# Kernel optimization log

Hardware: AMD Instinct MI355X
Metric: run time of the kernel (lower is better)

The kernel has to match this reference:

```python
import jax, jax.numpy as jnp
import numpy as np

# ---- constants matching init_kwargs ----
LAMBDA_CON = 0.4
LAMBDA_BC = 0.2
DX = 0.01
DT = 0.001
U0 = 1.0
VISC = 0.01
CROP = 512
N = CROP - 2  # 510
B = 32

# ---- fixed-weight convs expressed as slicing stencils (valid conv) ----
def div_ddx(x):      # 3x3 kernel [[0,0,0],[-1,1,0],[0,0,0]]
    return x[:, :, 1:-1, 1:-1] - x[:, :, 1:-1, :-2]

def div_ddy(x):      # 3x3 kernel [[0,-1,0],[0,1,0],[0,0,0]]
    return x[:, :, 1:-1, 1:-1] - x[:, :, :-2, 1:-1]

def avg_x(x):        # 2x2 kernel [[.5,.5],[0,0]]
    return 0.5 * (x[:, :, :-1, :-1] + x[:, :, :-1, 1:])

def avg_y(x):        # 2x2 kernel [[.5,0],[.5,0]]
    return 0.5 * (x[:, :, :-1, :-1] + x[:, :, 1:, :-1])

def up_ddx(x):       # 2x2 kernel [[-1,1],[0,0]]
    return x[:, :, :-1, 1:] - x[:, :, :-1, :-1]

def up_ddy(x):       # 2x2 kernel [[-1,0],[1,0]]
    return x[:, :, 1:, :-1] - x[:, :, :-1, :-1]

def down_ddx(x):     # 2x2 kernel [[0,0],[-1,1]]
    return x[:, :, 1:, 1:] - x[:, :, 1:, :-1]

def down_ddy(x):     # 2x2 kernel [[0,-1],[0,1]]
    return x[:, :, 1:, 1:] - x[:, :, :-1, 1:]

def laplacian(x):    # 3x3 kernel [[0,-1,0],[-1,4,-1],[0,-1,0]]
    return (4.0 * x[:, :, 1:-1, 1:-1]
            - x[:, :, 1:-1, 2:] - x[:, :, 1:-1, :-2]
            - x[:, :, 2:, 1:-1] - x[:, :, :-2, 1:-1])


def _poisson_dudt(u, v, p):
    ue = avg_x(u)
    vn = avg_x(v)
    flux_e = ue * avg_x(u) - (VISC / DX) * up_ddx(u)
    flux_n = vn * avg_y(u) - (VISC / DX) * up_ddy(u)
    flux_e = flux_e[:, :, :, :-1]
    flux_n = flux_n[:, :, :, :-1]
    pu = p[:, :, :-1, 1:-1]
    return (-down_ddx(flux_e) - down_ddy(flux_n) - down_ddx(pu)) / DX


def _poisson_dvdt(u, v, p):
    ue = avg_y(u)
    vn = avg_y(v)
    flux_e = ue * avg_x(v) - (VISC / DX) * up_ddx(v)
    flux_n = vn * avg_y(v) - (VISC / DX) * up_ddy(v)
    flux_e = flux_e[:, :, :-1, :]
    flux_n = flux_n[:, :, :-1, :]
    pv = p[:, :, 1:-1, :-1]
    return (-down_ddx(flux_e) - down_ddy(flux_n) - down_ddy(pv)) / DX


def _bc_loss(g):
    u, v, p = g[:, 0], g[:, 1], g[:, 2]  # [B,H,W]
    y0 = (jnp.sum(u[:, 0, 1:N] + u[:, 1, 1:N], axis=1)
          + jnp.sum(v[:, 0, 1:N + 1] + p[:, 0, 1:N + 1], axis=1))
    yL = (jnp.sum(2.0 * U0 - (u[:, N, 1:N] + u[:, N + 1, 1:N]), axis=1)
          + jnp.sum(v[:, N + 1, 1:N + 1] + p[:, N + 1, 1:N + 1], axis=1))
    x0 = (jnp.sum(v[:, 1:N, 0] + v[:, 1:N, 1], axis=1)
          + jnp.sum(u[:, 1:N + 1, 0] + p[:, 1:N + 1, 0], axis=1))
    xL = (jnp.sum(v[:, 1:N, N + 1] + v[:, 1:N, N], axis=1)
          + jnp.sum(u[:, 1:N + 1, N + 1] + p[:, 1:N + 1, N + 1], axis=1))
    return jnp.sum(jnp.abs(y0) + jnp.abs(yL) + jnp.abs(x0) + jnp.abs(xL))


def setup_inputs() -> dict:
    key = jax.random.key(0)
    k1, k2 = jax.random.split(key)
    gen_output = jax.random.normal(k1, (B, 3, CROP, CROP), dtype=jnp.float32)
    p_next_step = jax.random.normal(k2, (B, 1, CROP, CROP), dtype=jnp.float32)
    return {"gen_output": gen_output, "p_next_step": p_next_step}


def reference(gen_output, p_next_step):
    u = gen_output[:, 0:1]
    v = gen_output[:, 1:2]
    p = gen_output[:, 2:3]

    # continuity residual on interior grid [B,1,N,N]
    continuity_res = (div_ddx(u) + div_ddy(v)) / DX
    continuity_loss = jnp.mean(jnp.abs(continuity_res), axis=(2, 3))  # [B,1]

    dudt = _poisson_dudt(u, v, p)  # [B,1,N,N-1]
    dvdt = _poisson_dvdt(u, v, p)  # [B,1,N-1,N]
    dudt_pad = jnp.pad(dudt, ((0, 0), (0, 0), (1, 1), (1, 2)))  # -> [B,1,CROP,CROP]
    dvdt_pad = jnp.pad(dvdt, ((0, 0), (0, 0), (1, 2), (1, 1)))

    p_prime = p_next_step - p
    u_new = u + dudt_pad * DT
    v_new = v + dvdt_pad * DT
    b_conv = (div_ddx(u_new) / DX + div_ddy(v_new) / DX) / DT
    poisson_res = laplacian(p_prime) / DX ** 2 + b_conv  # [B,1,N,N]
    poisson_loss = jnp.mean(jnp.abs(poisson_res), axis=(2, 3))  # [B,1]

    b_c_loss = _bc_loss(gen_output)  # scalar

    pi_loss = (LAMBDA_CON * continuity_loss
               + LAMBDA_BC * b_c_loss
               + (1.0 - LAMBDA_CON - LAMBDA_BC) * poisson_loss)
    return jnp.mean(pi_loss)
```

## Files before the change

### kernel.cpp

```cpp
#include <hip/hip_runtime.h>

#define CROPX 512
#define NN 510
#define BATCHX 32

constexpr float INV_DX   = 100.0f;
constexpr float DT_F     = 0.001f;
constexpr float INV_DXDT = 100000.0f;
constexpr float INV_DX2  = 10000.0f;

#define IX(r,c) ((r)*CROPX + (c))

__global__ __launch_bounds__(256) void pde_main(const float* __restrict__ g,
                                                const float* __restrict__ png,
                                                float* __restrict__ ws) {
    const int bb   = blockIdx.z;
    const int tile = blockIdx.y;
    const int cg   = blockIdx.x;
    const int t    = threadIdx.x;
    const int lane = t & 63;

    const int borig  = cg * 256 + t;
    const bool active = (borig < NN);
    const int b = active ? borig : (NN - 1);

    const int a0 = tile * 32;
    const int a1 = (a0 + 32 < NN) ? (a0 + 32) : NN;

    const float* u  = g + (size_t)bb * 3 * (CROPX * CROPX);
    const float* v  = u + CROPX * CROPX;
    const float* p  = v + CROPX * CROPX;
    const float* pn = png + (size_t)bb * (CROPX * CROPX);

    float fnu_c, fnv_c, dvdt_c, ppN, ppC, v_up;
    {
        const int j = b + 1;
        float u_a_j  = u[IX(a0, j)];
        float u_a1_j = u[IX(a0 + 1, j)];
        float v_a_j  = v[IX(a0, j)];
        float v_a_j1 = v[IX(a0, j + 1)];
        float v_a1_j = v[IX(a0 + 1, j)];
        fnu_c = 0.5f * (v_a_j + v_a_j1) * 0.5f * (u_a_j + u_a1_j) - (u_a1_j - u_a_j);
        float vy = 0.5f * (v_a_j + v_a1_j);
        fnv_c = vy * vy - (v_a1_j - v_a_j);
        float p_a_j  = p[IX(a0, j)];
        float p_a1_j = p[IX(a0 + 1, j)];
        ppN = pn[IX(a0, j)] - p_a_j;
        ppC = pn[IX(a0 + 1, j)] - p_a1_j;
        v_up = v_a_j;
        dvdt_c = 0.0f;
        if (a0 > 0) {
            float u_a_b  = u[IX(a0, b)];
            float u_a1_b = u[IX(a0 + 1, b)];
            float v_a_b  = v[IX(a0, b)];
            float fev_b = 0.5f * (u_a_b + u_a1_b) * 0.5f * (v_a_b + v_a_j) - (v_a_j - v_a_b);
            float fev_j = 0.5f * (u_a_j + u_a1_j) * 0.5f * (v_a_j + v_a_j1) - (v_a_j1 - v_a_j);
            float v_am1_j = v[IX(a0 - 1, j)];
            float vym = 0.5f * (v_am1_j + v_a_j);
            float fnv_m = vym * vym - (v_a_j - v_am1_j);
            dvdt_c = (-(fev_j - fev_b) - (fnv_c - fnv_m) - (p_a1_j - p_a_j)) * INV_DX;
        }
    }

    float cont_acc = 0.0f, pois_acc = 0.0f;

    for (int a = a0; a < a1; ++a) {
        const int r1 = a + 1, r2 = a + 2;
        float u1_0 = u[IX(r1, b)],  u1_1 = u[IX(r1, b + 1)], u1_2 = u[IX(r1, b + 2)];
        float u2_0 = u[IX(r2, b)],  u2_1 = u[IX(r2, b + 1)];
        float v1_0 = v[IX(r1, b)],  v1_1 = v[IX(r1, b + 1)], v1_2 = v[IX(r1, b + 2)];
        float v2_1 = v[IX(r2, b + 1)];
        float p1_0 = p[IX(r1, b)],  p1_1 = p[IX(r1, b + 1)], p1_2 = p[IX(r1, b + 2)];
        float p2_1 = p[IX(r2, b + 1)];
        float pn1_0 = pn[IX(r1, b)], pn1_2 = pn[IX(r1, b + 2)], pn2_1 = pn[IX(r2, b + 1)];

        float ux_b  = 0.5f * (u1_0 + u1_1), ux_b1 = 0.5f * (u1_1 + u1_2);
        float feu_b  = ux_b  * ux_b  - (u1_1 - u1_0);
        float feu_b1 = ux_b1 * ux_b1 - (u1_2 - u1_1);
        float vx_b  = 0.5f * (v1_0 + v1_1), vx_b1 = 0.5f * (v1_1 + v1_2);
        float uy_b  = 0.5f * (u1_0 + u2_0), uy_b1 = 0.5f * (u1_1 + u2_1);
        float prod_b = uy_b * vx_b, prod_b1 = uy_b1 * vx_b1;
        float fnu_b1 = prod_b1 - (u2_1 - u1_1);
        float fev_b  = prod_b  - (v1_1 - v1_0);
        float fev_b1 = prod_b1 - (v1_2 - v1_1);
        float vy_b1 = 0.5f * (v1_1 + v2_1);
        float fnv_b1 = vy_b1 * vy_b1 - (v2_1 - v1_1);

        float dudt_b = (-(feu_b1 - feu_b) - (fnu_b1 - fnu_c) - (p1_2 - p1_1)) * INV_DX;
        float dvdt_b = (-(fev_b1 - fev_b) - (fnv_b1 - fnv_c) - (p2_1 - p1_1)) * INV_DX;

        float dudtL = __shfl_up(dudt_b, 1, 64);
        if (lane == 0 && b >= 1) {
            float um1 = u[IX(r1, b - 1)];
            float ux_m = 0.5f * (um1 + u1_0);
            float feu_m = ux_m * ux_m - (u1_0 - um1);
            float fnu_b0 = prod_b - (u2_0 - u1_0);
            float ua0 = u[IX(a, b)], va0 = v[IX(a, b)], va1 = v[IX(a, b + 1)];
            float fnu_a = 0.5f * (va0 + va1) * 0.5f * (ua0 + u1_0) - (u1_0 - ua0);
            dudtL = (-(feu_b - feu_m) - (fnu_b0 - fnu_a) - (p1_1 - p1_0)) * INV_DX;
        }

        float ppS = pn2_1 - p2_1;
        float ppW = pn1_0 - p1_0;
        float ppE = pn1_2 - p1_2;
        float lap = 4.0f * ppC - ppE - ppW - ppS - ppN;

        float du_x = u1_1 - u1_0;
        float dv_y = v1_1 - v_up;

        float dR = (b <= NN - 2) ? dudt_b : 0.0f;
        float dL = (b >= 1)      ? dudtL  : 0.0f;
        float vC = (a <= NN - 2) ? dvdt_b : 0.0f;
        float vP = (a >= 1)      ? dvdt_c : 0.0f;

        float bconv = (du_x + dv_y + DT_F * ((dR - dL) + (vC - vP))) * INV_DXDT;
        float pois  = lap * INV_DX2 + bconv;

        if (active) {
            cont_acc += fabsf((du_x + dv_y) * INV_DX);
            pois_acc += fabsf(pois);
        }

        fnu_c = fnu_b1; fnv_c = fnv_b1; dvdt_c = dvdt_b;
        ppN = ppC; ppC = ppS; v_up = v1_1;
    }

    __shared__ float sred[8];
    float c = cont_acc, q = pois_acc;
    for (int off = 32; off > 0; off >>= 1) {
        c += __shfl_down(c, off, 64);
        q += __shfl_down(q, off, 64);
    }
    int wid = t >> 6;
    if (lane == 0) { sred[wid] = c; sred[4 + wid] = q; }
    __syncthreads();
    if (t == 0) {
        float cs = sred[0] + sred[1] + sred[2] + sred[3];
        float qs = sred[4] + sred[5] + sred[6] + sred[7];
        atomicAdd(&ws[0], cs);
        atomicAdd(&ws[1], qs);
    }
}

__global__ __launch_bounds__(256) void pde_bc(const float* __restrict__ g,
                                              float* __restrict__ ws) {
    const int bb = blockIdx.x;
    const int t  = threadIdx.x;
    const int lane = t & 63;
    const float* u = g + (size_t)bb * 3 * (CROPX * CROPX);
    const float* v = u + CROPX * CROPX;
    const float* p = v + CROPX * CROPX;

    float y0 = 0.0f, yL = 0.0f, x0 = 0.0f, xL = 0.0f;
    for (int j = 1 + t; j <= NN; j += 256) {
        if (j <= NN - 1) {
            y0 += u[IX(0, j)] + u[IX(1, j)];
            yL += 2.0f - (u[IX(NN, j)] + u[IX(NN + 1, j)]);
            x0 += v[IX(j, 0)] + v[IX(j, 1)];
            xL += v[IX(j, CROPX - 1)] + v[IX(j, CROPX - 2)];
        }
        y0 += v[IX(0, j)] + p[IX(0, j)];
        yL += v[IX(NN + 1, j)] + p[IX(NN + 1, j)];
        x0 += u[IX(j, 0)] + p[IX(j, 0)];
        xL += u[IX(j, CROPX - 1)] + p[IX(j, CROPX - 1)];
    }

    __shared__ float s4[4][4];
    for (int off = 32; off > 0; off >>= 1) {
        y0 += __shfl_down(y0, off, 64);
        yL += __shfl_down(yL, off, 64);
        x0 += __shfl_down(x0, off, 64);
        xL += __shfl_down(xL, off, 64);
    }
    int wid = t >> 6;
    if (lane == 0) { s4[wid][0] = y0; s4[wid][1] = yL; s4[wid][2] = x0; s4[wid][3] = xL; }
    __syncthreads();
    if (t == 0) {
        float Y0 = s4[0][0] + s4[1][0] + s4[2][0] + s4[3][0];
        float YL = s4[0][1] + s4[1][1] + s4[2][1] + s4[3][1];
        float X0 = s4[0][2] + s4[1][2] + s4[2][2] + s4[3][2];
        float XL = s4[0][3] + s4[1][3] + s4[2][3] + s4[3][3];
        atomicAdd(&ws[2], fabsf(Y0) + fabsf(YL) + fabsf(X0) + fabsf(XL));
    }
}

__global__ void pde_final(const float* __restrict__ ws, float* __restrict__ out) {
    if (threadIdx.x == 0 && blockIdx.x == 0) {
        const float inv = 1.0f / (float)(BATCHX * NN * NN);
        out[0] = 0.4f * ws[0] * inv + 0.4f * ws[1] * inv + 0.2f * ws[2];
    }
}

extern "C" void kernel_launch(void* const* d_in, const int* in_sizes, int n_in,
                              void* d_out, int out_size, void* d_ws, size_t ws_size,
                              hipStream_t stream) {
    const float* g  = (const float*)d_in[0];
    const float* pn = (const float*)d_in[1];
    float* out = (float*)d_out;
    float* ws  = (float*)d_ws;

    hipMemsetAsync(ws, 0, 3 * sizeof(float), stream);

    dim3 grid(2, 16, 32);
    pde_main<<<grid, 256, 0, stream>>>(g, pn, ws);
    pde_bc<<<32, 256, 0, stream>>>(g, ws);
    pde_final<<<1, 64, 0, stream>>>(ws, out);
}
```

Before: 218.3 us.

## Vectorize stencil to 4 columns per thread with float4 loads and 8-row wave tiles

The main kernel now has each lane process four adjacent columns. It loads each row with one float4 plus two neighbour values taken by shuffle, and each wave handles an 8-row tile instead of a block walking 32 rows. The aim is fewer scalar global loads, more memory-level parallelism, and more rows in flight across 64 tiles per image. The boundary loss kernel is also parallelised across slices and roles, writing per-batch partial sums that the final kernel takes absolute values of and reduces. This raises register pressure from the unrolled loop and adds edge-lane special cases.

```diff
diff --git a/kernel.cpp b/kernel.cpp
--- a/kernel.cpp
+++ b/kernel.cpp
@@ -9,185 +9,226 @@
 constexpr float INV_DXDT = 100000.0f;
 constexpr float INV_DX2  = 10000.0f;
 
-#define IX(r,c) ((r)*CROPX + (c))
+__device__ __forceinline__ void load_row6(const float* __restrict__ base, int r,
+                                          int c0, int lane, float o[6]) {
+    const float* rp = base + (size_t)r * CROPX + c0;
+    const float4 q = *reinterpret_cast<const float4*>(rp);
+    float nx = __shfl_down(q.x, 1, 64);
+    float ny = __shfl_down(q.y, 1, 64);
+    if (lane == 63) {
+        const int lim = CROPX - 1 - c0;
+        nx = rp[4 < lim ? 4 : lim];
+        ny = rp[5 < lim ? 5 : lim];
+    }
+    o[0] = q.x; o[1] = q.y; o[2] = q.z; o[3] = q.w; o[4] = nx; o[5] = ny;
+}
 
 __global__ __launch_bounds__(256) void pde_main(const float* __restrict__ g,
                                                 const float* __restrict__ png,
                                                 float* __restrict__ ws) {
     const int bb   = blockIdx.z;
-    const int tile = blockIdx.y;
+    const int w    = threadIdx.x >> 6;
+    const int lane = threadIdx.x & 63;
+    const int tile = blockIdx.y * 4 + w;
     const int cg   = blockIdx.x;
-    const int t    = threadIdx.x;
-    const int lane = t & 63;
-
-    const int borig  = cg * 256 + t;
-    const bool active = (borig < NN);
-    const int b = active ? borig : (NN - 1);
-
-    const int a0 = tile * 32;
-    const int a1 = (a0 + 32 < NN) ? (a0 + 32) : NN;
+    const int c0   = cg * 256 + lane * 4;
+    const int a0   = tile * 8;
 
     const float* u  = g + (size_t)bb * 3 * (CROPX * CROPX);
     const float* v  = u + CROPX * CROPX;
     const float* p  = v + CROPX * CROPX;
     const float* pn = png + (size_t)bb * (CROPX * CROPX);
 
-    float fnu_c, fnv_c, dvdt_c, ppN, ppC, v_up;
+    const bool edgelane = (cg == 1 && lane == 0);
+
+    float u1[6], v1[6], p1[6], pn1[6];
+    float fnuC[5], fnvC[5], dvdtC[4], ppN[4], vup[4];
+
     {
-        const int j = b + 1;
-        float u_a_j  = u[IX(a0, j)];
-        float u_a1_j = u[IX(a0 + 1, j)];
-        float v_a_j  = v[IX(a0, j)];
-        float v_a_j1 = v[IX(a0, j + 1)];
-        float v_a1_j = v[IX(a0 + 1, j)];
-        fnu_c = 0.5f * (v_a_j + v_a_j1) * 0.5f * (u_a_j + u_a1_j) - (u_a1_j - u_a_j);
-        float vy = 0.5f * (v_a_j + v_a1_j);
-        fnv_c = vy * vy - (v_a1_j - v_a_j);
-        float p_a_j  = p[IX(a0, j)];
-        float p_a1_j = p[IX(a0 + 1, j)];
-        ppN = pn[IX(a0, j)] - p_a_j;
-        ppC = pn[IX(a0 + 1, j)] - p_a1_j;
-        v_up = v_a_j;
-        dvdt_c = 0.0f;
+        float ua[6], va[6], pa[6], pna[6];
+        load_row6(u,  a0, c0, lane, ua);
+        load_row6(v,  a0, c0, lane, va);
+        load_row6(p,  a0, c0, lane, pa);
+        load_row6(pn, a0, c0, lane, pna);
+        load_row6(u,  a0 + 1, c0, lane, u1);
+        load_row6(v,  a0 + 1, c0, lane, v1);
+        load_row6(p,  a0 + 1, c0, lane, p1);
+        load_row6(pn, a0 + 1, c0, lane, pn1);
+
+        #pragma unroll
+        for (int j = 0; j < 5; ++j)
+            fnuC[j] = 0.5f * (va[j] + va[j + 1]) * 0.5f * (ua[j] + u1[j]) - (u1[j] - ua[j]);
+        #pragma unroll
+        for (int j = 1; j < 5; ++j) {
+            float m = 0.5f * (va[j] + v1[j]);
+            fnvC[j] = m * m - (v1[j] - va[j]);
+        }
+        #pragma unroll
+        for (int k = 0; k < 4; ++k) { ppN[k] = pna[k + 1] - pa[k + 1]; vup[k] = va[k + 1]; }
+
         if (a0 > 0) {
-            float u_a_b  = u[IX(a0, b)];
-            float u_a1_b = u[IX(a0 + 1, b)];
-            float v_a_b  = v[IX(a0, b)];
-            float fev_b = 0.5f * (u_a_b + u_a1_b) * 0.5f * (v_a_b + v_a_j) - (v_a_j - v_a_b);
-            float fev_j = 0.5f * (u_a_j + u_a1_j) * 0.5f * (v_a_j + v_a_j1) - (v_a_j1 - v_a_j);
-            float v_am1_j = v[IX(a0 - 1, j)];
-            float vym = 0.5f * (v_am1_j + v_a_j);
-            float fnv_m = vym * vym - (v_a_j - v_am1_j);
-            dvdt_c = (-(fev_j - fev_b) - (fnv_c - fnv_m) - (p_a1_j - p_a_j)) * INV_DX;
+            float vm[6];
+            load_row6(v, a0 - 1, c0, lane, vm);
+            float fev[5];
+            #pragma unroll
+            for (int j = 0; j < 5; ++j)
+                fev[j] = 0.5f * (ua[j] + u1[j]) * 0.5f * (va[j] + va[j + 1]) - (va[j + 1] - va[j]);
+            #pragma unroll
+            for (int k = 0; k < 4; ++k) {
+                float mm = 0.5f * (vm[k + 1] + va[k + 1]);
+                float fnvm = mm * mm - (va[k + 1] - vm[k + 1]);
+                dvdtC[k] = (-(fev[k + 1] - fev[k]) - (fnvC[k + 1] - fnvm)
+                            - (p1[k + 1] - pa[k + 1])) * INV_DX;
+            }
+        } else {
+            #pragma unroll
+            for (int k = 0; k < 4; ++k) dvdtC[k] = 0.0f;
         }
     }
 
     float cont_acc = 0.0f, pois_acc = 0.0f;
 
-    for (int a = a0; a < a1; ++a) {
-        const int r1 = a + 1, r2 = a + 2;
-        float u1_0 = u[IX(r1, b)],  u1_1 = u[IX(r1, b + 1)], u1_2 = u[IX(r1, b + 2)];
-        float u2_0 = u[IX(r2, b)],  u2_1 = u[IX(r2, b + 1)];
-        float v1_0 = v[IX(r1, b)],  v1_1 = v[IX(r1, b + 1)], v1_2 = v[IX(r1, b + 2)];
-        float v2_1 = v[IX(r2, b + 1)];
-        float p1_0 = p[IX(r1, b)],  p1_1 = p[IX(r1, b + 1)], p1_2 = p[IX(r1, b + 2)];
-        float p2_1 = p[IX(r2, b + 1)];
-        float pn1_0 = pn[IX(r1, b)], pn1_2 = pn[IX(r1, b + 2)], pn2_1 = pn[IX(r2, b + 1)];
-
-        float ux_b  = 0.5f * (u1_0 + u1_1), ux_b1 = 0.5f * (u1_1 + u1_2);
-        float feu_b  = ux_b  * ux_b  - (u1_1 - u1_0);
-        float feu_b1 = ux_b1 * ux_b1 - (u1_2 - u1_1);
-        float vx_b  = 0.5f * (v1_0 + v1_1), vx_b1 = 0.5f * (v1_1 + v1_2);
-        float uy_b  = 0.5f * (u1_0 + u2_0), uy_b1 = 0.5f * (u1_1 + u2_1);
-        float prod_b = uy_b * vx_b, prod_b1 = uy_b1 * vx_b1;
-        float fnu_b1 = prod_b1 - (u2_1 - u1_1);
-        float fev_b  = prod_b  - (v1_1 - v1_0);
-        float fev_b1 = prod_b1 - (v1_2 - v1_1);
-        float vy_b1 = 0.5f * (v1_1 + v2_1);
-        float fnv_b1 = vy_b1 * vy_b1 - (v2_1 - v1_1);
-
-        float dudt_b = (-(feu_b1 - feu_b) - (fnu_b1 - fnu_c) - (p1_2 - p1_1)) * INV_DX;
-        float dvdt_b = (-(fev_b1 - fev_b) - (fnv_b1 - fnv_c) - (p2_1 - p1_1)) * INV_DX;
-
-        float dudtL = __shfl_up(dudt_b, 1, 64);
-        if (lane == 0 && b >= 1) {
-            float um1 = u[IX(r1, b - 1)];
-            float ux_m = 0.5f * (um1 + u1_0);
-            float feu_m = ux_m * ux_m - (u1_0 - um1);
-            float fnu_b0 = prod_b - (u2_0 - u1_0);
-            float ua0 = u[IX(a, b)], va0 = v[IX(a, b)], va1 = v[IX(a, b + 1)];
-            float fnu_a = 0.5f * (va0 + va1) * 0.5f * (ua0 + u1_0) - (u1_0 - ua0);
-            dudtL = (-(feu_b - feu_m) - (fnu_b0 - fnu_a) - (p1_1 - p1_0)) * INV_DX;
-        }
-
-        float ppS = pn2_1 - p2_1;
-        float ppW = pn1_0 - p1_0;
-        float ppE = pn1_2 - p1_2;
-        float lap = 4.0f * ppC - ppE - ppW - ppS - ppN;
-
-        float du_x = u1_1 - u1_0;
-        float dv_y = v1_1 - v_up;
-
-        float dR = (b <= NN - 2) ? dudt_b : 0.0f;
-        float dL = (b >= 1)      ? dudtL  : 0.0f;
-        float vC = (a <= NN - 2) ? dvdt_b : 0.0f;
-        float vP = (a >= 1)      ? dvdt_c : 0.0f;
-
-        float bconv = (du_x + dv_y + DT_F * ((dR - dL) + (vC - vP))) * INV_DXDT;
-        float pois  = lap * INV_DX2 + bconv;
-
-        if (active) {
-            cont_acc += fabsf((du_x + dv_y) * INV_DX);
-            pois_acc += fabsf(pois);
-        }
-
-        fnu_c = fnu_b1; fnv_c = fnv_b1; dvdt_c = dvdt_b;
-        ppN = ppC; ppC = ppS; v_up = v1_1;
-    }
-
-    __shared__ float sred[8];
+    #pragma unroll
+    for (int it = 0; it < 8; ++it) {
+        const int a  = a0 + it;
+        const int r1 = (a + 1 < CROPX) ? a + 1 : CROPX - 1;
+        const int r2 = (a + 2 < CROPX) ? a + 2 : CROPX - 1;
+
+        float u2[6], v2[6], p2[6], pn2[6];
+        load_row6(u,  r2, c0, lane, u2);
+        load_row6(v,  r2, c0, lane, v2);
+        load_row6(p,  r2, c0, lane, p2);
+        load_row6(pn, r2, c0, lane, pn2);
+
+        float uLeft = 0.0f;
+        if (edgelane) uLeft = u[(size_t)r1 * CROPX + (c0 - 1)];
+
+        float FEu[5], FEv[5], FNu1[5], FNv1[5];
+        #pragma unroll
+        for (int j = 0; j < 5; ++j) {
+            float ux = 0.5f * (u1[j] + u1[j + 1]);
+            FEu[j] = ux * ux - (u1[j + 1] - u1[j]);
+            float uy = 0.5f * (u1[j] + u2[j]);
+            float vx = 0.5f * (v1[j] + v1[j + 1]);
+            float prod = uy * vx;
+            FEv[j]  = prod - (v1[j + 1] - v1[j]);
+            FNu1[j] = prod - (u2[j] - u1[j]);
+        }
+        #pragma unroll
+        for (int j = 1; j < 5; ++j) {
+            float vy = 0.5f * (v1[j] + v2[j]);
+            FNv1[j] = vy * vy - (v2[j] - v1[j]);
+        }
+
+        float dudt[4], dvdt[4];
+        #pragma unroll
+        for (int k = 0; k < 4; ++k) {
+            dudt[k] = (-(FEu[k + 1] - FEu[k]) - (FNu1[k + 1] - fnuC[k + 1])
+                       - (p1[k + 2] - p1[k + 1])) * INV_DX;
+            dvdt[k] = (-(FEv[k + 1] - FEv[k]) - (FNv1[k + 1] - fnvC[k + 1])
+                       - (p2[k + 1] - p1[k + 1])) * INV_DX;
+        }
+
+        float dudtLm = __shfl_up(dudt[3], 1, 64);
+        if (edgelane) {
+            float uxm  = 0.5f * (uLeft + u1[0]);
+            float FEuL = uxm * uxm - (u1[0] - uLeft);
+            dudtLm = (-(FEu[0] - FEuL) - (FNu1[0] - fnuC[0]) - (p1[1] - p1[0])) * INV_DX;
+        }
+
+        #pragma unroll
+        for (int k = 0; k < 4; ++k) {
+            const int b = c0 + k;
+            float ppC = pn1[k + 1] - p1[k + 1];
+            float ppS = pn2[k + 1] - p2[k + 1];
+            float ppW = pn1[k]     - p1[k];
+            float ppE = pn1[k + 2] - p1[k + 2];
+            float lap = 4.0f * ppC - ppE - ppW - ppS - ppN[k];
+            float du_x = u1[k + 1] - u1[k];
+            float dv_y = v1[k + 1] - vup[k];
+            float dL  = (k == 0) ? dudtLm : dudt[k - 1];
+            float dRm = (b <= NN - 2) ? dudt[k] : 0.0f;
+            float dLm = (b >= 1)      ? dL      : 0.0f;
+            float vCm = (a <= NN - 2) ? dvdt[k] : 0.0f;
+            float vPm = (a >= 1)      ? dvdtC[k] : 0.0f;
+            float bconv = (du_x + dv_y + DT_F * ((dRm - dLm) + (vCm - vPm))) * INV_DXDT;
+            float pois  = lap * INV_DX2 + bconv;
+            if (b < NN && a < NN) {
+                cont_acc += fabsf((du_x + dv_y) * INV_DX);
+                pois_acc += fabsf(pois);
+            }
+            ppN[k]   = ppC;
+            vup[k]   = v1[k + 1];
+            dvdtC[k] = dvdt[k];
+        }
+        #pragma unroll
+        for (int j = 0; j < 5; ++j) { fnuC[j] = FNu1[j]; if (j >= 1) fnvC[j] = FNv1[j]; }
+        #pragma unroll
+        for (int j = 0; j < 6; ++j) { u1[j] = u2[j]; v1[j] = v2[j]; p1[j] = p2[j]; pn1[j] = pn2[j]; }
+    }
+
     float c = cont_acc, q = pois_acc;
+    #pragma unroll
     for (int off = 32; off > 0; off >>= 1) {
         c += __shfl_down(c, off, 64);
         q += __shfl_down(q, off, 64);
     }
-    int wid = t >> 6;
-    if (lane == 0) { sred[wid] = c; sred[4 + wid] = q; }
+    __shared__ float sred[8];
+    if (lane == 0) { sred[w] = c; sred[4 + w] = q; }
     __syncthreads();
-    if (t == 0) {
-        float cs = sred[0] + sred[1] + sred[2] + sred[3];
-        float qs = sred[4] + sred[5] + sred[6] + sred[7];
-        atomicAdd(&ws[0], cs);
-        atomicAdd(&ws[1], qs);
+    if (threadIdx.x == 0) {
+        atomicAdd(&ws[0], sred[0] + sred[1] + sred[2] + sred[3]);
+        atomicAdd(&ws[1], sred[4] + sred[5] + sred[6] + sred[7]);
     }
 }
 
 __global__ __launch_bounds__(256) void pde_bc(const float* __restrict__ g,
                                               float* __restrict__ ws) {
-    const int bb = blockIdx.x;
-    const int t  = threadIdx.x;
-    const int lane = t & 63;
+    const int bb    = blockIdx.y;
+    const int slice = blockIdx.x;
+    const int lane  = threadIdx.x & 63;
+    const int role  = threadIdx.x >> 6;
+    const int j     = slice * 64 + lane;
+
     const float* u = g + (size_t)bb * 3 * (CROPX * CROPX);
     const float* v = u + CROPX * CROPX;
     const float* p = v + CROPX * CROPX;
 
-    float y0 = 0.0f, yL = 0.0f, x0 = 0.0f, xL = 0.0f;
-    for (int j = 1 + t; j <= NN; j += 256) {
-        if (j <= NN - 1) {
-            y0 += u[IX(0, j)] + u[IX(1, j)];
-            yL += 2.0f - (u[IX(NN, j)] + u[IX(NN + 1, j)]);
-            x0 += v[IX(j, 0)] + v[IX(j, 1)];
-            xL += v[IX(j, CROPX - 1)] + v[IX(j, CROPX - 2)];
-        }
-        y0 += v[IX(0, j)] + p[IX(0, j)];
-        yL += v[IX(NN + 1, j)] + p[IX(NN + 1, j)];
-        x0 += u[IX(j, 0)] + p[IX(j, 0)];
-        xL += u[IX(j, CROPX - 1)] + p[IX(j, CROPX - 1)];
-    }
-
-    __shared__ float s4[4][4];
-    for (int off = 32; off > 0; off >>= 1) {
-        y0 += __shfl_down(y0, off, 64);
-        yL += __shfl_down(yL, off, 64);
-        x0 += __shfl_down(x0, off, 64);
-        xL += __shfl_down(xL, off, 64);
-    }
-    int wid = t >> 6;
-    if (lane == 0) { s4[wid][0] = y0; s4[wid][1] = yL; s4[wid][2] = x0; s4[wid][3] = xL; }
-    __syncthreads();
+    const bool in9  = (j >= 1 && j <= NN - 1);
+    const bool in10 = (j >= 1 && j <= NN);
+
+    float val = 0.0f;
+    if (role == 0) {
+        if (in9)  val += u[j] + u[CROPX + j];
+        if (in10) val += v[j] + p[j];
+    } else if (role == 1) {
+        if (in9)  val += 2.0f - u[(size_t)NN * CROPX + j] - u[(size_t)(NN + 1) * CROPX + j];
+        if (in10) val += v[(size_t)(NN + 1) * CROPX + j] + p[(size_t)(NN + 1) * CROPX + j];
+    } else if (role == 2) {
+        if (in9)  val += v[(size_t)j * CROPX] + v[(size_t)j * CROPX + 1];
+        if (in10) val += u[(size_t)j * CROPX] + p[(size_t)j * CROPX];
+    } else {
+        if (in9)  val += v[(size_t)j * CROPX + (CROPX - 1)] + v[(size_t)j * CROPX + (CROPX - 2)];
+        if (in10) val += u[(size_t)j * CROPX + (CROPX - 1)] + p[(size_t)j * CROPX + (CROPX - 1)];
+    }
+
+    #pragma unroll
+    for (int off = 32; off > 0; off >>= 1) val += __shfl_down(val, off, 64);
+    if (lane == 0) atomicAdd(&ws[4 + bb * 4 + role], val);
+}
+
+__global__ void pde_final(const float* __restrict__ ws, float* __restrict__ out) {
+    const int t = threadIdx.x;
+    float bc = 0.0f;
+    if (t < BATCHX) {
+        const float* wb = ws + 4 + t * 4;
+        bc = fabsf(wb[0]) + fabsf(wb[1]) + fabsf(wb[2]) + fabsf(wb[3]);
+    }
+    #pragma unroll
+    for (int off = 32; off > 0; off >>= 1) bc += __shfl_down(bc, off, 64);
     if (t == 0) {
-        float Y0 = s4[0][0] + s4[1][0] + s4[2][0] + s4[3][0];
-        float YL = s4[0][1] + s4[1][1] + s4[2][1] + s4[3][1];
-        float X0 = s4[0][2] + s4[1][2] + s4[2][2] + s4[3][2];
-        float XL = s4[0][3] + s4[1][3] + s4[2][3] + s4[3][3];
-        atomicAdd(&ws[2], fabsf(Y0) + fabsf(YL) + fabsf(X0) + fabsf(XL));
-    }
-}
-
-__global__ void pde_final(const float* __restrict__ ws, float* __restrict__ out) {
-    if (threadIdx.x == 0 && blockIdx.x == 0) {
-        const float inv = 1.0f / (float)(BATCHX * NN * NN);
-        out[0] = 0.4f * ws[0] * inv + 0.4f * ws[1] * inv + 0.2f * ws[2];
+        const float inv = 1.0f / ((float)BATCHX * NN * NN);
+        out[0] = 0.4f * (ws[0] + ws[1]) * inv + 0.2f * bc;
     }
 }
 
@@ -199,10 +240,11 @@
     float* out = (float*)d_out;
     float* ws  = (float*)d_ws;
 
-    hipMemsetAsync(ws, 0, 3 * sizeof(float), stream);
-
-    dim3 grid(2, 16, 32);
-    pde_main<<<grid, 256, 0, stream>>>(g, pn, ws);
-    pde_bc<<<32, 256, 0, stream>>>(g, ws);
+    hipMemsetAsync(ws, 0, (4 + BATCHX * 4) * sizeof(float), stream);
+
+    dim3 gm(2, 16, 32);
+    pde_main<<<gm, 256, 0, stream>>>(g, pn, ws);
+    dim3 gb(8, 32);
+    pde_bc<<<gb, 256, 0, stream>>>(g, ws);
     pde_final<<<1, 64, 0, stream>>>(ws, out);
 }
```

Result: no change. 219.4 us (+0.5%).
